# Performance work log

Hardware: AMD Instinct MI355X
Metric: run time of the kernel (lower is better)

## Reference

```python
import jax, jax.numpy as jnp
import numpy as np


def fake_quant(x):
    # Per-tensor symmetric int8 fake quantization with straight-through estimator.
    scale = jnp.maximum(jnp.max(jnp.abs(x)) / 127.0, 1e-8)
    q = jnp.clip(jnp.round(x / scale), -128.0, 127.0) * scale
    return x + jax.lax.stop_gradient(q - x)


def setup_inputs() -> dict:
    key = jax.random.key(0)
    k = jax.random.split(key, 6)
    B, R, M0, M1, OUT = 8192, 64, 64, 64, 4096
    return {
        "x0": jax.random.normal(k[0], (B, M0), dtype=jnp.float32),
        "x1": jax.random.normal(k[1], (B, M1), dtype=jnp.float32),
        "f0": jax.random.normal(k[2], (M0, R), dtype=jnp.float32) * 0.1,
        "f1": jax.random.normal(k[3], (M1, R), dtype=jnp.float32) * 0.1,
        "f2": jax.random.normal(k[4], (OUT, R), dtype=jnp.float32) * 0.1,
        "bias": jnp.full((OUT,), 0.1, dtype=jnp.float32),
    }


def reference(x0, x1, f0, f1, f2, bias):
    # CP factor matmul chain with elementwise (Hadamard) fusion over modes
    out = (x0 @ fake_quant(f0)) * (x1 @ fake_quant(f1))  # [B, R]
    out = out @ fake_quant(f2).T                          # [B, OUT]
    out = fake_quant(out + bias)
    return jax.nn.relu(out)
```

## Files before the change

kernel.cpp:

```cpp
#include <hip/hip_runtime.h>
#include <math.h>

#define NB   8192
#define NR   64
#define NOUT 4096

typedef __attribute__((ext_vector_type(8))) short bf16x8;
typedef __attribute__((ext_vector_type(4))) float f32x4;


static constexpr size_t OFF_FC2  = 256;
static constexpr size_t OFF_FC0T = OFF_FC2  + 256 * 2048;
static constexpr size_t OFF_FC1T = OFF_FC0T + 4 * 2048;
static constexpr size_t OFF_FX0H = OFF_FC1T + 4 * 2048;
static constexpr size_t OFF_FX0L = OFF_FX0H + 512 * 2048;
static constexpr size_t OFF_FX1H = OFF_FX0L + 512 * 2048;
static constexpr size_t OFF_FX1L = OFF_FX1H + 512 * 2048;
static constexpr size_t OFF_FTH  = OFF_FX1L + 512 * 2048;
static constexpr size_t OFF_FTL  = OFF_FTH  + 512 * 2048;
static constexpr size_t OFF_BMAX = OFF_FTL  + 512 * 2048;

__device__ __forceinline__ float wave_max(float v) {
#pragma unroll
  for (int off = 32; off > 0; off >>= 1) v = fmaxf(v, __shfl_down(v, off));
  return v;
}

__device__ __forceinline__ unsigned short f2bf(float f) {
  unsigned u = __float_as_uint(f);
  unsigned r = u + 0x7fff + ((u >> 16) & 1);
  return (unsigned short)(r >> 16);
}
__device__ __forceinline__ float bf2f(unsigned short h) {
  return __uint_as_float(((unsigned)h) << 16);
}
__device__ __forceinline__ float fq_scale(unsigned bits) {
  return fmaxf(__uint_as_float(bits) / 127.0f, 1e-8f);
}
__device__ __forceinline__ float qcode(float x, float sinv) {
  return fminf(fmaxf(rintf(x * sinv), -128.0f), 127.0f);
}

__device__ __forceinline__ int ft_idx(int row, int k) {
  return (row >> 4) * 1024 + (k >> 5) * 512 +
         ((row & 15) + (((k & 31) >> 3) << 4)) * 8 + (k & 7);
}

__global__ __launch_bounds__(256) void absmax_factors(
    const float* __restrict__ f0, const float* __restrict__ f1,
    const float* __restrict__ f2, unsigned* __restrict__ slots) {
  __shared__ float wred[4];
  int bid = blockIdx.x, tid = threadIdx.x;
  const float* src;
  int slot, i4;
  if (bid < 256)      { src = f2; slot = 2; i4 = bid * 256 + tid; }
  else if (bid < 260) { src = f0; slot = 0; i4 = (bid - 256) * 256 + tid; }
  else                { src = f1; slot = 1; i4 = (bid - 260) * 256 + tid; }
  float4 v = ((const float4*)src)[i4];
  float a = fmaxf(fmaxf(fabsf(v.x), fabsf(v.y)), fmaxf(fabsf(v.z), fabsf(v.w)));
  a = wave_max(a);
  if ((tid & 63) == 0) wred[tid >> 6] = a;
  __syncthreads();
  if (tid == 0) {
    float m = fmaxf(fmaxf(wred[0], wred[1]), fmaxf(wred[2], wred[3]));
    atomicMax(&slots[slot], __float_as_uint(m));
  }
}

__global__ __launch_bounds__(256) void prep(
    const float* __restrict__ f0, const float* __restrict__ f1,
    const float* __restrict__ f2, const float* __restrict__ x0,
    const float* __restrict__ x1, const unsigned* __restrict__ slots,
    unsigned short* __restrict__ fc0t, unsigned short* __restrict__ fc1t,
    unsigned short* __restrict__ fc2, unsigned short* __restrict__ fx0h,
    unsigned short* __restrict__ fx0l, unsigned short* __restrict__ fx1h,
    unsigned short* __restrict__ fx1l) {
  int bid = blockIdx.x, tid = threadIdx.x;
  if (bid < 256) {
    float sinv = 1.0f / fq_scale(slots[2]);
    int i4 = bid * 256 + tid;
    int e = i4 * 4, m = e >> 6, r0 = e & 63;
    float4 v = ((const float4*)f2)[i4];
    unsigned short c0 = f2bf(qcode(v.x, sinv)), c1 = f2bf(qcode(v.y, sinv));
    unsigned short cc2 = f2bf(qcode(v.z, sinv)), c3 = f2bf(qcode(v.w, sinv));
    uint2 p;
    p.x = (unsigned)c0 | ((unsigned)c1 << 16);
    p.y = (unsigned)cc2 | ((unsigned)c3 << 16);
    *(uint2*)(fc2 + ft_idx(m, r0)) = p;
  } else if (bid < 1280) {
    const float* x = (bid < 768) ? x0 : x1;
    unsigned short* xh = (bid < 768) ? fx0h : fx1h;
    unsigned short* xl = (bid < 768) ? fx0l : fx1l;
    int i4 = ((bid < 768) ? (bid - 256) : (bid - 768)) * 256 + tid;
    int e = i4 * 4, m = e >> 6, r0 = e & 63;
    float4 v = ((const float4*)x)[i4];
    float vv[4] = {v.x, v.y, v.z, v.w};
    unsigned short h[4], lo[4];
#pragma unroll
    for (int j = 0; j < 4; ++j) {
      h[j] = f2bf(vv[j]);
      lo[j] = f2bf(vv[j] - bf2f(h[j]));
    }
    uint2 ph, pl;
    ph.x = (unsigned)h[0] | ((unsigned)h[1] << 16);
    ph.y = (unsigned)h[2] | ((unsigned)h[3] << 16);
    pl.x = (unsigned)lo[0] | ((unsigned)lo[1] << 16);
    pl.y = (unsigned)lo[2] | ((unsigned)lo[3] << 16);
    int idx = ft_idx(m, r0);
    *(uint2*)(xh + idx) = ph;
    *(uint2*)(xl + idx) = pl;
  } else {
    const float* f = (bid < 1284) ? f0 : f1;
    unsigned short* ct = (bid < 1284) ? fc0t : fc1t;
    float sinv = 1.0f / fq_scale(slots[(bid < 1284) ? 0 : 1]);
    int i4 = ((bid < 1284) ? (bid - 1280) : (bid - 1284)) * 256 + tid;
    int e = i4 * 4, m = e >> 6, r0 = e & 63;
    float4 v = ((const float4*)f)[i4];
    float vv[4] = {v.x, v.y, v.z, v.w};
#pragma unroll
    for (int q = 0; q < 4; ++q)
      ct[ft_idx(r0 + q, m)] = f2bf(qcode(vv[q], sinv));
  }
}

__global__ __launch_bounds__(256) void stage1(
    const unsigned short* __restrict__ fx0h, const unsigned short* __restrict__ fx0l,
    const unsigned short* __restrict__ fx1h, const unsigned short* __restrict__ fx1l,
    const unsigned short* __restrict__ fc0t, const unsigned short* __restrict__ fc1t,
    const unsigned* __restrict__ slots,
    unsigned short* __restrict__ fth, unsigned short* __restrict__ ftl) {
  int tid = threadIdx.x;
  int l = tid & 63, nf = tid >> 6;
  int t = blockIdx.x;
  int abase = t * 1024 + l * 8;

  bf16x8 a0h0 = *(const bf16x8*)(fx0h + abase), a0h1 = *(const bf16x8*)(fx0h + abase + 512);
  bf16x8 a0l0 = *(const bf16x8*)(fx0l + abase), a0l1 = *(const bf16x8*)(fx0l + abase + 512);
  bf16x8 a1h0 = *(const bf16x8*)(fx1h + abase), a1h1 = *(const bf16x8*)(fx1h + abase + 512);
  bf16x8 a1l0 = *(const bf16x8*)(fx1l + abase), a1l1 = *(const bf16x8*)(fx1l + abase + 512);

  int bbase = nf * 1024 + l * 8;
  bf16x8 b0a = *(const bf16x8*)(fc0t + bbase), b0b = *(const bf16x8*)(fc0t + bbase + 512);
  bf16x8 b1a = *(const bf16x8*)(fc1t + bbase), b1b = *(const bf16x8*)(fc1t + bbase + 512);

  f32x4 acc0 = {}, acc1 = {};
  acc0 = __builtin_amdgcn_mfma_f32_16x16x32_bf16(a0h0, b0a, acc0, 0, 0, 0);
  acc0 = __builtin_amdgcn_mfma_f32_16x16x32_bf16(a0l0, b0a, acc0, 0, 0, 0);
  acc0 = __builtin_amdgcn_mfma_f32_16x16x32_bf16(a0h1, b0b, acc0, 0, 0, 0);
  acc0 = __builtin_amdgcn_mfma_f32_16x16x32_bf16(a0l1, b0b, acc0, 0, 0, 0);
  acc1 = __builtin_amdgcn_mfma_f32_16x16x32_bf16(a1h0, b1a, acc1, 0, 0, 0);
  acc1 = __builtin_amdgcn_mfma_f32_16x16x32_bf16(a1l0, b1a, acc1, 0, 0, 0);
  acc1 = __builtin_amdgcn_mfma_f32_16x16x32_bf16(a1h1, b1b, acc1, 0, 0, 0);
  acc1 = __builtin_amdgcn_mfma_f32_16x16x32_bf16(a1l1, b1b, acc1, 0, 0, 0);

  float s01 = fq_scale(slots[0]) * fq_scale(slots[1]);
#pragma unroll
  for (int j = 0; j < 4; ++j) {
    float tv = s01 * acc0[j] * acc1[j];
    int row_in = (l >> 4) * 4 + j;
    int r = nf * 16 + (l & 15);
    int idx = t * 1024 + (r >> 5) * 512 +
              (row_in + (((r & 31) >> 3) << 4)) * 8 + (r & 7);
    unsigned short h = f2bf(tv);
    fth[idx] = h;
    ftl[idx] = f2bf(tv - bf2f(h));
  }
}

template <int MODE>
__global__ __launch_bounds__(256) void stage2(
    const unsigned short* __restrict__ fth, const unsigned short* __restrict__ ftl,
    const unsigned short* __restrict__ fc2, const float* __restrict__ bias,
    const unsigned* __restrict__ slots, float* __restrict__ bmax,
    const unsigned* __restrict__ absmaxY, float* __restrict__ out) {
  __shared__ float wred[4];
  int tid = threadIdx.x;
  int wid = tid >> 6, l = tid & 63;
  int m0 = blockIdx.y * 256 + wid * 64;
  int n0 = blockIdx.x * 64;
  int mt0 = m0 >> 4, nt0 = n0 >> 4;
  float s2 = fq_scale(slots[2]);

  bf16x8 bfr[4][2];
#pragma unroll
  for (int nf = 0; nf < 4; ++nf) {
    int bb = (nt0 + nf) * 1024 + l * 8;
    bfr[nf][0] = *(const bf16x8*)(fc2 + bb);
    bfr[nf][1] = *(const bf16x8*)(fc2 + bb + 512);
  }

  f32x4 acc[4][4] = {};
#pragma unroll
  for (int mf = 0; mf < 4; ++mf) {
    int ab = (mt0 + mf) * 1024 + l * 8;
    bf16x8 ah0 = *(const bf16x8*)(fth + ab), ah1 = *(const bf16x8*)(fth + ab + 512);
    bf16x8 al0 = *(const bf16x8*)(ftl + ab), al1 = *(const bf16x8*)(ftl + ab + 512);
#pragma unroll
    for (int nf = 0; nf < 4; ++nf) {
      acc[mf][nf] = __builtin_amdgcn_mfma_f32_16x16x32_bf16(ah0, bfr[nf][0], acc[mf][nf], 0, 0, 0);
      acc[mf][nf] = __builtin_amdgcn_mfma_f32_16x16x32_bf16(al0, bfr[nf][0], acc[mf][nf], 0, 0, 0);
      acc[mf][nf] = __builtin_amdgcn_mfma_f32_16x16x32_bf16(ah1, bfr[nf][1], acc[mf][nf], 0, 0, 0);
      acc[mf][nf] = __builtin_amdgcn_mfma_f32_16x16x32_bf16(al1, bfr[nf][1], acc[mf][nf], 0, 0, 0);
    }
  }

  float bs[4];
#pragma unroll
  for (int nf = 0; nf < 4; ++nf) bs[nf] = bias[n0 + nf * 16 + (l & 15)];

  if (MODE == 0) {
    float m = 0.0f;
#pragma unroll
    for (int mf = 0; mf < 4; ++mf)
#pragma unroll
      for (int nf = 0; nf < 4; ++nf)
#pragma unroll
        for (int j = 0; j < 4; ++j)
          m = fmaxf(m, fabsf(s2 * acc[mf][nf][j] + bs[nf]));
    m = wave_max(m);
    if ((tid & 63) == 0) wred[tid >> 6] = m;
    __syncthreads();
    if (tid == 0) {
      float mm = fmaxf(fmaxf(wred[0], wred[1]), fmaxf(wred[2], wred[3]));
      bmax[blockIdx.y * gridDim.x + blockIdx.x] = mm;
    }
  } else {
    float sY = fq_scale(*absmaxY);
    float inv = 1.0f / sY;
#pragma unroll
    for (int mf = 0; mf < 4; ++mf) {
      int r0 = m0 + mf * 16 + (l >> 4) * 4;
#pragma unroll
      for (int nf = 0; nf < 4; ++nf) {
        int c = n0 + nf * 16 + (l & 15);
#pragma unroll
        for (int j = 0; j < 4; ++j) {
          float v = s2 * acc[mf][nf][j] + bs[nf];
          float q = fminf(fmaxf(rintf(v * inv), -128.0f), 127.0f) * sY;
          out[(size_t)(r0 + j) * NOUT + c] = fmaxf(q, 0.0f);
        }
      }
    }
  }
}

__global__ __launch_bounds__(256) void reduce_bmax(
    const float* __restrict__ bmax, unsigned* __restrict__ slot) {
  __shared__ float wred[4];
  int tid = threadIdx.x;
  float m = 0.0f;
#pragma unroll
  for (int i = 0; i < 8; ++i) m = fmaxf(m, bmax[tid + i * 256]);
  m = wave_max(m);
  if ((tid & 63) == 0) wred[tid >> 6] = m;
  __syncthreads();
  if (tid == 0) {
    float mm = fmaxf(fmaxf(wred[0], wred[1]), fmaxf(wred[2], wred[3]));
    *slot = __float_as_uint(mm);
  }
}

extern "C" void kernel_launch(void* const* d_in, const int* in_sizes, int n_in,
                              void* d_out, int out_size, void* d_ws,
                              size_t ws_size, hipStream_t stream) {
  (void)in_sizes; (void)n_in; (void)out_size; (void)ws_size;
  const float* x0 = (const float*)d_in[0];
  const float* x1 = (const float*)d_in[1];
  const float* f0 = (const float*)d_in[2];
  const float* f1 = (const float*)d_in[3];
  const float* f2 = (const float*)d_in[4];
  const float* bias = (const float*)d_in[5];
  float* out = (float*)d_out;

  char* ws = (char*)d_ws;
  unsigned* slots = (unsigned*)ws;
  unsigned short* fc2  = (unsigned short*)(ws + OFF_FC2);
  unsigned short* fc0t = (unsigned short*)(ws + OFF_FC0T);
  unsigned short* fc1t = (unsigned short*)(ws + OFF_FC1T);
  unsigned short* fx0h = (unsigned short*)(ws + OFF_FX0H);
  unsigned short* fx0l = (unsigned short*)(ws + OFF_FX0L);
  unsigned short* fx1h = (unsigned short*)(ws + OFF_FX1H);
  unsigned short* fx1l = (unsigned short*)(ws + OFF_FX1L);
  unsigned short* fth  = (unsigned short*)(ws + OFF_FTH);
  unsigned short* ftl  = (unsigned short*)(ws + OFF_FTL);
  float* bmax = (float*)(ws + OFF_BMAX);

  hipMemsetAsync(d_ws, 0, 256, stream);
  absmax_factors<<<264, 256, 0, stream>>>(f0, f1, f2, slots);
  prep<<<1288, 256, 0, stream>>>(f0, f1, f2, x0, x1, slots, fc0t, fc1t, fc2,
                                 fx0h, fx0l, fx1h, fx1l);
  stage1<<<512, 256, 0, stream>>>(fx0h, fx0l, fx1h, fx1l, fc0t, fc1t, slots,
                                  fth, ftl);
  stage2<0><<<dim3(64, 32), 256, 0, stream>>>(fth, ftl, fc2, bias, slots,
                                              bmax, nullptr, nullptr);
  reduce_bmax<<<1, 256, 0, stream>>>(bmax, slots + 3);
  stage2<1><<<dim3(64, 32), 256, 0, stream>>>(fth, ftl, fc2, bias, slots,
                                              nullptr, slots + 3, out);
}
```

Before: 174.7 us.

## Fuse x bf16 split and factor quantization into stage1, drop memset and atomics

Stage1 now reads x0/x1 directly and splits them into bf16 hi/lo in registers, and each block recomputes the f0/f1 absmax and quantized factor tiles into shared memory. This removes the prep pass that wrote and re-read the split x buffers. The f2 absmax uses per-block partials plus a second kernel instead of atomics, so the memset is gone. Stage2 blocks are remapped so the 32 M-tiles are spread evenly across the 8 XCDs for better L2 locality. The cost is redundant factor quantization in every stage1 block and extra LDS use.

```diff
diff --git a/kernel.cpp b/kernel.cpp
--- a/kernel.cpp
+++ b/kernel.cpp
@@ -9,16 +9,11 @@
 typedef __attribute__((ext_vector_type(4))) float f32x4;
 
 
-static constexpr size_t OFF_FC2  = 256;
-static constexpr size_t OFF_FC0T = OFF_FC2  + 256 * 2048;
-static constexpr size_t OFF_FC1T = OFF_FC0T + 4 * 2048;
-static constexpr size_t OFF_FX0H = OFF_FC1T + 4 * 2048;
-static constexpr size_t OFF_FX0L = OFF_FX0H + 512 * 2048;
-static constexpr size_t OFF_FX1H = OFF_FX0L + 512 * 2048;
-static constexpr size_t OFF_FX1L = OFF_FX1H + 512 * 2048;
-static constexpr size_t OFF_FTH  = OFF_FX1L + 512 * 2048;
-static constexpr size_t OFF_FTL  = OFF_FTH  + 512 * 2048;
-static constexpr size_t OFF_BMAX = OFF_FTL  + 512 * 2048;
+static constexpr size_t OFF_PF2  = 256;
+static constexpr size_t OFF_BMAX = 2048;
+static constexpr size_t OFF_FC2  = 16384;
+static constexpr size_t OFF_FTH  = OFF_FC2 + 256 * 2048;
+static constexpr size_t OFF_FTL  = OFF_FTH + (size_t)512 * 2048 * 2;
 
 __device__ __forceinline__ float wave_max(float v) {
 #pragma unroll
@@ -34,9 +29,6 @@
 __device__ __forceinline__ float bf2f(unsigned short h) {
   return __uint_as_float(((unsigned)h) << 16);
 }
-__device__ __forceinline__ float fq_scale(unsigned bits) {
-  return fmaxf(__uint_as_float(bits) / 127.0f, 1e-8f);
-}
 __device__ __forceinline__ float qcode(float x, float sinv) {
   return fminf(fmaxf(rintf(x * sinv), -128.0f), 127.0f);
 }
@@ -46,102 +38,112 @@
          ((row & 15) + (((k & 31) >> 3) << 4)) * 8 + (k & 7);
 }
 
-__global__ __launch_bounds__(256) void absmax_factors(
-    const float* __restrict__ f0, const float* __restrict__ f1,
-    const float* __restrict__ f2, unsigned* __restrict__ slots) {
-  __shared__ float wred[4];
-  int bid = blockIdx.x, tid = threadIdx.x;
-  const float* src;
-  int slot, i4;
-  if (bid < 256)      { src = f2; slot = 2; i4 = bid * 256 + tid; }
-  else if (bid < 260) { src = f0; slot = 0; i4 = (bid - 256) * 256 + tid; }
-  else                { src = f1; slot = 1; i4 = (bid - 260) * 256 + tid; }
-  float4 v = ((const float4*)src)[i4];
+__device__ __forceinline__ void split8(float4 a, float4 b, bf16x8& h, bf16x8& lo) {
+  float v[8] = {a.x, a.y, a.z, a.w, b.x, b.y, b.z, b.w};
+#pragma unroll
+  for (int j = 0; j < 8; ++j) {
+    unsigned short hh = f2bf(v[j]);
+    h[j] = (short)hh;
+    lo[j] = (short)f2bf(v[j] - bf2f(hh));
+  }
+}
+
+__global__ __launch_bounds__(256) void absmax_f2(
+    const float* __restrict__ f2, float* __restrict__ pf2) {
+  __shared__ float wred[4];
+  int tid = threadIdx.x;
+  float4 v = ((const float4*)f2)[blockIdx.x * 256 + tid];
   float a = fmaxf(fmaxf(fabsf(v.x), fabsf(v.y)), fmaxf(fabsf(v.z), fabsf(v.w)));
   a = wave_max(a);
   if ((tid & 63) == 0) wred[tid >> 6] = a;
   __syncthreads();
-  if (tid == 0) {
-    float m = fmaxf(fmaxf(wred[0], wred[1]), fmaxf(wred[2], wred[3]));
-    atomicMax(&slots[slot], __float_as_uint(m));
-  }
-}
-
-__global__ __launch_bounds__(256) void prep(
+  if (tid == 0)
+    pf2[blockIdx.x] = fmaxf(fmaxf(wred[0], wred[1]), fmaxf(wred[2], wred[3]));
+}
+
+__global__ __launch_bounds__(256) void prep_f2(
+    const float* __restrict__ f2, const float* __restrict__ pf2,
+    float* __restrict__ slots_f, unsigned short* __restrict__ fc2) {
+  __shared__ float wred[4];
+  int tid = threadIdx.x, bid = blockIdx.x;
+  float a = pf2[tid];
+  a = wave_max(a);
+  if ((tid & 63) == 0) wred[tid >> 6] = a;
+  __syncthreads();
+  float am = fmaxf(fmaxf(wred[0], wred[1]), fmaxf(wred[2], wred[3]));
+  float s2 = fmaxf(am * (1.0f / 127.0f), 1e-8f);
+  if (bid == 0 && tid == 0) slots_f[2] = s2;
+  float sinv = 1.0f / s2;
+  int i4 = bid * 256 + tid;
+  int e = i4 * 4, m = e >> 6, r0 = e & 63;
+  float4 v = ((const float4*)f2)[i4];
+  unsigned short c0 = f2bf(qcode(v.x, sinv)), c1 = f2bf(qcode(v.y, sinv));
+  unsigned short cc2 = f2bf(qcode(v.z, sinv)), c3 = f2bf(qcode(v.w, sinv));
+  uint2 p;
+  p.x = (unsigned)c0 | ((unsigned)c1 << 16);
+  p.y = (unsigned)cc2 | ((unsigned)c3 << 16);
+  *(uint2*)(fc2 + ft_idx(m, r0)) = p;
+}
+
+__global__ __launch_bounds__(256) void stage1_fused(
+    const float* __restrict__ x0, const float* __restrict__ x1,
     const float* __restrict__ f0, const float* __restrict__ f1,
-    const float* __restrict__ f2, const float* __restrict__ x0,
-    const float* __restrict__ x1, const unsigned* __restrict__ slots,
-    unsigned short* __restrict__ fc0t, unsigned short* __restrict__ fc1t,
-    unsigned short* __restrict__ fc2, unsigned short* __restrict__ fx0h,
-    unsigned short* __restrict__ fx0l, unsigned short* __restrict__ fx1h,
-    unsigned short* __restrict__ fx1l) {
-  int bid = blockIdx.x, tid = threadIdx.x;
-  if (bid < 256) {
-    float sinv = 1.0f / fq_scale(slots[2]);
-    int i4 = bid * 256 + tid;
-    int e = i4 * 4, m = e >> 6, r0 = e & 63;
-    float4 v = ((const float4*)f2)[i4];
-    unsigned short c0 = f2bf(qcode(v.x, sinv)), c1 = f2bf(qcode(v.y, sinv));
-    unsigned short cc2 = f2bf(qcode(v.z, sinv)), c3 = f2bf(qcode(v.w, sinv));
-    uint2 p;
-    p.x = (unsigned)c0 | ((unsigned)c1 << 16);
-    p.y = (unsigned)cc2 | ((unsigned)c3 << 16);
-    *(uint2*)(fc2 + ft_idx(m, r0)) = p;
-  } else if (bid < 1280) {
-    const float* x = (bid < 768) ? x0 : x1;
-    unsigned short* xh = (bid < 768) ? fx0h : fx1h;
-    unsigned short* xl = (bid < 768) ? fx0l : fx1l;
-    int i4 = ((bid < 768) ? (bid - 256) : (bid - 768)) * 256 + tid;
-    int e = i4 * 4, m = e >> 6, r0 = e & 63;
-    float4 v = ((const float4*)x)[i4];
-    float vv[4] = {v.x, v.y, v.z, v.w};
-    unsigned short h[4], lo[4];
+    unsigned short* __restrict__ fth, unsigned short* __restrict__ ftl) {
+  __shared__ float wred0[4], wred1[4];
+  __shared__ unsigned short c0s[4096], c1s[4096];
+  int tid = threadIdx.x;
+
+  float a0 = 0.0f, a1 = 0.0f;
+#pragma unroll
+  for (int i = 0; i < 4; ++i) {
+    float4 v0 = ((const float4*)f0)[tid + i * 256];
+    float4 v1 = ((const float4*)f1)[tid + i * 256];
+    a0 = fmaxf(a0, fmaxf(fmaxf(fabsf(v0.x), fabsf(v0.y)),
+                         fmaxf(fabsf(v0.z), fabsf(v0.w))));
+    a1 = fmaxf(a1, fmaxf(fmaxf(fabsf(v1.x), fabsf(v1.y)),
+                         fmaxf(fabsf(v1.z), fabsf(v1.w))));
+  }
+  a0 = wave_max(a0);
+  a1 = wave_max(a1);
+  if ((tid & 63) == 0) { wred0[tid >> 6] = a0; wred1[tid >> 6] = a1; }
+  __syncthreads();
+  float am0 = fmaxf(fmaxf(wred0[0], wred0[1]), fmaxf(wred0[2], wred0[3]));
+  float am1 = fmaxf(fmaxf(wred1[0], wred1[1]), fmaxf(wred1[2], wred1[3]));
+  float s0 = fmaxf(am0 * (1.0f / 127.0f), 1e-8f);
+  float s1 = fmaxf(am1 * (1.0f / 127.0f), 1e-8f);
+  float sinv0 = 1.0f / s0, sinv1 = 1.0f / s1;
+
+  int m = tid >> 2, rb = (tid & 3) * 16;
+#pragma unroll
+  for (int i = 0; i < 4; ++i) {
+    float4 v0 = ((const float4*)f0)[tid * 4 + i];
+    float4 v1 = ((const float4*)f1)[tid * 4 + i];
+    float w0[4] = {v0.x, v0.y, v0.z, v0.w};
+    float w1[4] = {v1.x, v1.y, v1.z, v1.w};
 #pragma unroll
     for (int j = 0; j < 4; ++j) {
-      h[j] = f2bf(vv[j]);
-      lo[j] = f2bf(vv[j] - bf2f(h[j]));
-    }
-    uint2 ph, pl;
-    ph.x = (unsigned)h[0] | ((unsigned)h[1] << 16);
-    ph.y = (unsigned)h[2] | ((unsigned)h[3] << 16);
-    pl.x = (unsigned)lo[0] | ((unsigned)lo[1] << 16);
-    pl.y = (unsigned)lo[2] | ((unsigned)lo[3] << 16);
-    int idx = ft_idx(m, r0);
-    *(uint2*)(xh + idx) = ph;
-    *(uint2*)(xl + idx) = pl;
-  } else {
-    const float* f = (bid < 1284) ? f0 : f1;
-    unsigned short* ct = (bid < 1284) ? fc0t : fc1t;
-    float sinv = 1.0f / fq_scale(slots[(bid < 1284) ? 0 : 1]);
-    int i4 = ((bid < 1284) ? (bid - 1280) : (bid - 1284)) * 256 + tid;
-    int e = i4 * 4, m = e >> 6, r0 = e & 63;
-    float4 v = ((const float4*)f)[i4];
-    float vv[4] = {v.x, v.y, v.z, v.w};
-#pragma unroll
-    for (int q = 0; q < 4; ++q)
-      ct[ft_idx(r0 + q, m)] = f2bf(qcode(vv[q], sinv));
-  }
-}
-
-__global__ __launch_bounds__(256) void stage1(
-    const unsigned short* __restrict__ fx0h, const unsigned short* __restrict__ fx0l,
-    const unsigned short* __restrict__ fx1h, const unsigned short* __restrict__ fx1l,
-    const unsigned short* __restrict__ fc0t, const unsigned short* __restrict__ fc1t,
-    const unsigned* __restrict__ slots,
-    unsigned short* __restrict__ fth, unsigned short* __restrict__ ftl) {
-  int tid = threadIdx.x;
+      int r = rb + i * 4 + j;
+      c0s[ft_idx(r, m)] = f2bf(qcode(w0[j], sinv0));
+      c1s[ft_idx(r, m)] = f2bf(qcode(w1[j], sinv1));
+    }
+  }
+  __syncthreads();
+
   int l = tid & 63, nf = tid >> 6;
-  int t = blockIdx.x;
-  int abase = t * 1024 + l * 8;
-
-  bf16x8 a0h0 = *(const bf16x8*)(fx0h + abase), a0h1 = *(const bf16x8*)(fx0h + abase + 512);
-  bf16x8 a0l0 = *(const bf16x8*)(fx0l + abase), a0l1 = *(const bf16x8*)(fx0l + abase + 512);
-  bf16x8 a1h0 = *(const bf16x8*)(fx1h + abase), a1h1 = *(const bf16x8*)(fx1h + abase + 512);
-  bf16x8 a1l0 = *(const bf16x8*)(fx1l + abase), a1l1 = *(const bf16x8*)(fx1l + abase + 512);
-
-  int bbase = nf * 1024 + l * 8;
-  bf16x8 b0a = *(const bf16x8*)(fc0t + bbase), b0b = *(const bf16x8*)(fc0t + bbase + 512);
-  bf16x8 b1a = *(const bf16x8*)(fc1t + bbase), b1b = *(const bf16x8*)(fc1t + bbase + 512);
+  int b0 = blockIdx.x * 16;
+  int row = b0 + (l & 15), kb = (l >> 4) * 8;
+  const float* p0 = x0 + (size_t)row * 64 + kb;
+  const float* p1 = x1 + (size_t)row * 64 + kb;
+  bf16x8 a0h0, a0l0, a0h1, a0l1, a1h0, a1l0, a1h1, a1l1;
+  split8(*(const float4*)p0, *(const float4*)(p0 + 4), a0h0, a0l0);
+  split8(*(const float4*)(p0 + 32), *(const float4*)(p0 + 36), a0h1, a0l1);
+  split8(*(const float4*)p1, *(const float4*)(p1 + 4), a1h0, a1l0);
+  split8(*(const float4*)(p1 + 32), *(const float4*)(p1 + 36), a1h1, a1l1);
+
+  bf16x8 b0a = *(const bf16x8*)(c0s + nf * 1024 + l * 8);
+  bf16x8 b0b = *(const bf16x8*)(c0s + nf * 1024 + l * 8 + 512);
+  bf16x8 b1a = *(const bf16x8*)(c1s + nf * 1024 + l * 8);
+  bf16x8 b1b = *(const bf16x8*)(c1s + nf * 1024 + l * 8 + 512);
 
   f32x4 acc0 = {}, acc1 = {};
   acc0 = __builtin_amdgcn_mfma_f32_16x16x32_bf16(a0h0, b0a, acc0, 0, 0, 0);
@@ -153,13 +155,13 @@
   acc1 = __builtin_amdgcn_mfma_f32_16x16x32_bf16(a1h1, b1b, acc1, 0, 0, 0);
   acc1 = __builtin_amdgcn_mfma_f32_16x16x32_bf16(a1l1, b1b, acc1, 0, 0, 0);
 
-  float s01 = fq_scale(slots[0]) * fq_scale(slots[1]);
+  float s01 = s0 * s1;
 #pragma unroll
   for (int j = 0; j < 4; ++j) {
     float tv = s01 * acc0[j] * acc1[j];
     int row_in = (l >> 4) * 4 + j;
     int r = nf * 16 + (l & 15);
-    int idx = t * 1024 + (r >> 5) * 512 +
+    int idx = blockIdx.x * 1024 + (r >> 5) * 512 +
               (row_in + (((r & 31) >> 3) << 4)) * 8 + (r & 7);
     unsigned short h = f2bf(tv);
     fth[idx] = h;
@@ -171,15 +173,19 @@
 __global__ __launch_bounds__(256) void stage2(
     const unsigned short* __restrict__ fth, const unsigned short* __restrict__ ftl,
     const unsigned short* __restrict__ fc2, const float* __restrict__ bias,
-    const unsigned* __restrict__ slots, float* __restrict__ bmax,
-    const unsigned* __restrict__ absmaxY, float* __restrict__ out) {
-  __shared__ float wred[4];
+    const float* __restrict__ slots_f, float* __restrict__ bmax,
+    float* __restrict__ out) {
+  __shared__ float wred[4];
+  int flat = blockIdx.x;
+  int xcd = flat & 7, local = flat >> 3;
+  int mt = xcd * 4 + (local >> 6);
+  int nt = local & 63;
   int tid = threadIdx.x;
   int wid = tid >> 6, l = tid & 63;
-  int m0 = blockIdx.y * 256 + wid * 64;
-  int n0 = blockIdx.x * 64;
+  int m0 = mt * 256 + wid * 64;
+  int n0 = nt * 64;
   int mt0 = m0 >> 4, nt0 = n0 >> 4;
-  float s2 = fq_scale(slots[2]);
+  float s2 = slots_f[2];
 
   bf16x8 bfr[4][2];
 #pragma unroll
@@ -221,11 +227,10 @@
     if ((tid & 63) == 0) wred[tid >> 6] = m;
     __syncthreads();
     if (tid == 0) {
-      float mm = fmaxf(fmaxf(wred[0], wred[1]), fmaxf(wred[2], wred[3]));
-      bmax[blockIdx.y * gridDim.x + blockIdx.x] = mm;
+      bmax[flat] = fmaxf(fmaxf(wred[0], wred[1]), fmaxf(wred[2], wred[3]));
     }
   } else {
-    float sY = fq_scale(*absmaxY);
+    float sY = slots_f[3];
     float inv = 1.0f / sY;
 #pragma unroll
     for (int mf = 0; mf < 4; ++mf) {
@@ -245,7 +250,7 @@
 }
 
 __global__ __launch_bounds__(256) void reduce_bmax(
-    const float* __restrict__ bmax, unsigned* __restrict__ slot) {
+    const float* __restrict__ bmax, float* __restrict__ slots_f) {
   __shared__ float wred[4];
   int tid = threadIdx.x;
   float m = 0.0f;
@@ -256,7 +261,7 @@
   __syncthreads();
   if (tid == 0) {
     float mm = fmaxf(fmaxf(wred[0], wred[1]), fmaxf(wred[2], wred[3]));
-    *slot = __float_as_uint(mm);
+    slots_f[3] = fmaxf(mm * (1.0f / 127.0f), 1e-8f);
   }
 }
 
@@ -273,27 +278,19 @@
   float* out = (float*)d_out;
 
   char* ws = (char*)d_ws;
-  unsigned* slots = (unsigned*)ws;
-  unsigned short* fc2  = (unsigned short*)(ws + OFF_FC2);
-  unsigned short* fc0t = (unsigned short*)(ws + OFF_FC0T);
-  unsigned short* fc1t = (unsigned short*)(ws + OFF_FC1T);
-  unsigned short* fx0h = (unsigned short*)(ws + OFF_FX0H);
-  unsigned short* fx0l = (unsigned short*)(ws + OFF_FX0L);
-  unsigned short* fx1h = (unsigned short*)(ws + OFF_FX1H);
-  unsigned short* fx1l = (unsigned short*)(ws + OFF_FX1L);
-  unsigned short* fth  = (unsigned short*)(ws + OFF_FTH);
-  unsigned short* ftl  = (unsigned short*)(ws + OFF_FTL);
+  float* slots_f = (float*)ws;
+  float* pf2  = (float*)(ws + OFF_PF2);
   float* bmax = (float*)(ws + OFF_BMAX);
-
-  hipMemsetAsync(d_ws, 0, 256, stream);
-  absmax_factors<<<264, 256, 0, stream>>>(f0, f1, f2, slots);
-  prep<<<1288, 256, 0, stream>>>(f0, f1, f2, x0, x1, slots, fc0t, fc1t, fc2,
-                                 fx0h, fx0l, fx1h, fx1l);
-  stage1<<<512, 256, 0, stream>>>(fx0h, fx0l, fx1h, fx1l, fc0t, fc1t, slots,
-                                  fth, ftl);
-  stage2<0><<<dim3(64, 32), 256, 0, stream>>>(fth, ftl, fc2, bias, slots,
-                                              bmax, nullptr, nullptr);
-  reduce_bmax<<<1, 256, 0, stream>>>(bmax, slots + 3);
-  stage2<1><<<dim3(64, 32), 256, 0, stream>>>(fth, ftl, fc2, bias, slots,
-                                              nullptr, slots + 3, out);
-}
+  unsigned short* fc2 = (unsigned short*)(ws + OFF_FC2);
+  unsigned short* fth = (unsigned short*)(ws + OFF_FTH);
+  unsigned short* ftl = (unsigned short*)(ws + OFF_FTL);
+
+  absmax_f2<<<256, 256, 0, stream>>>(f2, pf2);
+  prep_f2<<<256, 256, 0, stream>>>(f2, pf2, slots_f, fc2);
+  stage1_fused<<<512, 256, 0, stream>>>(x0, x1, f0, f1, fth, ftl);
+  stage2<0><<<2048, 256, 0, stream>>>(fth, ftl, fc2, bias, slots_f, bmax,
+                                      nullptr);
+  reduce_bmax<<<1, 256, 0, stream>>>(bmax, slots_f);
+  stage2<1><<<2048, 256, 0, stream>>>(fth, ftl, fc2, bias, slots_f, nullptr,
+                                      out);
+}
```

Measured after the change: 170.7 us. 2.3% less time.
